# Optimization experiments

Measured on AMD Instinct MI355X. Metric: run time of the kernel, lower is better.

The kernel has to match this reference:

```python
import jax, jax.numpy as jnp
import numpy as np
from jax import lax

ANCHOR_AREAS = (128.0**2, 256.0**2, 512.0**2)
ASPECT_RATIOS = (0.5, 1.0, 2.0)
STRIDE = 32.0                      # resnet backbone: get_orig_stat maps fm -> input via x*32
PRE_NMS_TOP_N = 2000
POST_NMS_TOP_N = 100
NMS_IOU_T = 0.7
SCORE_T = 0.1
MIN_SCALE = 0.01
BBOX_XFORM_CLIP = float(np.log(1000.0 / 16.0))


def make_anchors(H, W):
    # anchors laid out in (H, W, A) order to match the offset permutation below
    sizes = []
    for area in ANCHOR_AREAS:
        for r in ASPECT_RATIOS:          # aspect_ratio = w / h
            sizes.append((np.sqrt(area * r), np.sqrt(area / r)))
    sizes = jnp.asarray(np.asarray(sizes, dtype=np.float32))  # [A, 2] (w, h)
    cy = (jnp.arange(H, dtype=jnp.float32) + 0.5) * STRIDE
    cx = (jnp.arange(W, dtype=jnp.float32) + 0.5) * STRIDE
    cyg, cxg = jnp.meshgrid(cy, cx, indexing='ij')             # [H, W]
    cxg = cxg[:, :, None]
    cyg = cyg[:, :, None]
    w = sizes[:, 0]
    h = sizes[:, 1]
    anchors = jnp.stack([cxg - w / 2, cyg - h / 2, cxg + w / 2, cyg + h / 2], axis=-1)
    return anchors.reshape(-1, 4)                              # [H*W*A, 4] xyxy


def decode_boxes(anchors, offsets):
    # anchors [N,4], offsets [B,N,4] (tx, ty, tw, th) -> boxes [B,N,4] xyxy
    wa = anchors[:, 2] - anchors[:, 0]
    ha = anchors[:, 3] - anchors[:, 1]
    cxa = anchors[:, 0] + 0.5 * wa
    cya = anchors[:, 1] + 0.5 * ha
    tx, ty = offsets[..., 0], offsets[..., 1]
    tw = jnp.minimum(offsets[..., 2], BBOX_XFORM_CLIP)
    th = jnp.minimum(offsets[..., 3], BBOX_XFORM_CLIP)
    px = tx * wa + cxa
    py = ty * ha + cya
    pw = jnp.exp(tw) * wa
    ph = jnp.exp(th) * ha
    return jnp.stack([px - pw / 2, py - ph / 2, px + pw / 2, py + ph / 2], axis=-1)


def box_iou(a, b):
    area_a = (a[:, 2] - a[:, 0]) * (a[:, 3] - a[:, 1])
    area_b = (b[:, 2] - b[:, 0]) * (b[:, 3] - b[:, 1])
    lt = jnp.maximum(a[:, None, :2], b[None, :, :2])
    rb = jnp.minimum(a[:, None, 2:], b[None, :, 2:])
    wh = jnp.clip(rb - lt, 0.0)
    inter = wh[..., 0] * wh[..., 1]
    return inter / (area_a[:, None] + area_b[None, :] - inter + 1e-9)


def nms_single(boxes, scores):
    # boxes [P,4] sorted by descending score; invalid entries carry score -1
    P = boxes.shape[0]
    iou = box_iou(boxes, boxes)
    idx = jnp.arange(P)

    def body(i, keep):
        sup = (iou[i] > NMS_IOU_T) & (idx > i)
        return jnp.where(keep[i], keep & (~sup), keep)

    keep = lax.stop_gradient(lax.fori_loop(0, P, body, scores > 0.0))
    kept_scores = jnp.where(keep, scores, -1.0)
    top_s, top_i = lax.top_k(kept_scores, POST_NMS_TOP_N)
    return boxes[top_i], top_s


def rpn_forward(features, W1, b1, W2, b2, W3, b3):
    B, Cin, H, W = features.shape
    A = W3.shape[0]
    # 3x3 sliding conv + ReLU
    t = lax.conv_general_dilated(
        features, W1, window_strides=(1, 1), padding='SAME',
        dimension_numbers=('NCHW', 'OIHW', 'NCHW'))
    t = jax.nn.relu(t + b1[None, :, None, None])
    # 1x1 sibling heads as channel contractions
    offs = jnp.einsum('bchw,oc->bohw', t, W2) + b2[None, :, None, None]   # [B, A*4, H, W]
    logits = jnp.einsum('bchw,oc->bohw', t, W3) + b3[None, :, None, None]  # [B, A, H, W]
    # reorder to per-anchor layout (H, W, A)
    offs = offs.reshape(B, A, 4, H, W).transpose(0, 3, 4, 1, 2).reshape(B, -1, 4)
    scores = jax.nn.sigmoid(logits.transpose(0, 2, 3, 1).reshape(B, -1))  # [B, N]
    anchors = make_anchors(H, W)
    boxes = decode_boxes(anchors, offs)                                    # [B, N, 4]
    # clip to image boundary (handle_cross_boundary_boxes during testing)
    img_w, img_h = W * STRIDE, H * STRIDE
    boxes = jnp.stack([
        jnp.clip(boxes[..., 0], 0.0, img_w),
        jnp.clip(boxes[..., 1], 0.0, img_h),
        jnp.clip(boxes[..., 2], 0.0, img_w),
        jnp.clip(boxes[..., 3], 0.0, img_h)], axis=-1)
    # score-threshold + min-scale filtering
    bw = boxes[..., 2] - boxes[..., 0]
    bh = boxes[..., 3] - boxes[..., 1]
    valid = (scores >= SCORE_T) & (bw > MIN_SCALE * img_w) & (bh > MIN_SCALE * img_h)
    masked = jnp.where(valid, scores, -1.0)
    # pre-NMS top-k, then per-image NMS + post-NMS top-n
    top_s, top_i = lax.top_k(masked, PRE_NMS_TOP_N)                        # [B, P]
    top_boxes = jnp.take_along_axis(boxes, top_i[..., None], axis=1)       # [B, P, 4]
    out_boxes, out_scores = jax.vmap(nms_single)(top_boxes, top_s)
    return out_boxes, out_scores                                           # [B,100,4], [B,100]


def setup_inputs() -> dict:
    key = jax.random.key(0)
    ks = jax.random.split(key, 4)
    B, Cin, H, W = 8, 1024, 50, 50
    A = 9
    C = 512
    return {
        'features': jax.random.normal(ks[0], (B, Cin, H, W), jnp.float32),
        'W1': jax.random.normal(ks[1], (C, Cin, 3, 3), jnp.float32) * 0.01,
        'b1': jnp.zeros((C,), jnp.float32),
        'W2': jax.random.normal(ks[2], (A * 4, C), jnp.float32) * 0.01,
        'b2': jnp.zeros((A * 4,), jnp.float32),
        'W3': jax.random.normal(ks[3], (A, C), jnp.float32) * 0.01,
        'b3': jnp.zeros((A,), jnp.float32),
    }


def reference(features, W1, b1, W2, b2, W3, b3):
    return rpn_forward(features, W1, b1, W2, b2, W3, b3)
```

## Files before the change

### kernel.cpp

```cpp
#include <hip/hip_runtime.h>
#include <cstdint>

#define NB 8
#define CIN 1024
#define HDIM 50
#define WDIM 50
#define COUT 512
#define NA 9
#define NANCH (HDIM*WDIM*NA)
#define PRE_N 2000
#define POST_N 100

typedef __attribute__((ext_vector_type(8))) short bf16x8;
typedef __attribute__((ext_vector_type(4))) float f32x4;
typedef __attribute__((ext_vector_type(16))) float f32x16;
typedef __attribute__((ext_vector_type(8))) unsigned short ushort8v;

constexpr size_t TPLANE    = 20578304;
constexpr size_t OFF_TPH   = 0;
constexpr size_t OFF_TPL   = 20578304;
constexpr size_t OFF_BOXES = 41156608;
constexpr size_t OFF_KEYS  = 44036608;
constexpr size_t OFF_TBOX  = 45476608;
constexpr size_t OFF_TS    = 45732608;
constexpr size_t OFF_SUP   = 45796608;
constexpr size_t QDIM      = 2976;
constexpr size_t PLSTRIDE  = QDIM * 8;
constexpr size_t PPLANE    = 48758784;
constexpr size_t OFF_PH    = 49892864;
constexpr size_t OFF_PL    = OFF_PH + PPLANE;
constexpr size_t WPLANE    = 9437184;
constexpr size_t OFF_WH    = 147410432;
constexpr size_t OFF_WL    = OFF_WH + WPLANE;

__device__ __forceinline__ void split2bf16(float v, unsigned short &hi, unsigned short &lo) {
    unsigned int u = __float_as_uint(v);
    unsigned int r = u + 0x7FFFu + ((u >> 16) & 1u);
    hi = (unsigned short)(r >> 16);
    float hf = __uint_as_float(((unsigned int)hi) << 16);
    float lf = v - hf;
    unsigned int u2 = __float_as_uint(lf);
    unsigned int r2 = u2 + 0x7FFFu + ((u2 >> 16) & 1u);
    lo = (unsigned short)(r2 >> 16);
}

__device__ __forceinline__ void gl_lds(const unsigned short* g, unsigned short* l) {
    __builtin_amdgcn_global_load_lds(
        (const __attribute__((address_space(1))) unsigned int*)(const void*)g,
        (__attribute__((address_space(3))) unsigned int*)(void*)l,
        16, 0, 0);
}

__global__ __launch_bounds__(256) void prep_all(const float* __restrict__ f,
                                                const float* __restrict__ W1,
                                                unsigned short* __restrict__ Ph,
                                                unsigned short* __restrict__ Pl,
                                                unsigned short* __restrict__ Wh,
                                                unsigned short* __restrict__ Wl) {
    int blk = blockIdx.x;
    if (blk < 5952) {
        int id = blk * 256 + threadIdx.x;
        int q = id % (int)QDIM; int r = id / (int)QDIM;
        int cic = r % 64; int b = r / 64;
        int pp = q - 53;
        int rr = pp / 52, cc = pp - rr * 52;
        int h = rr - 1, w = cc - 1;
        bool inb = (pp >= 0) && (pp < 2704) && (h >= 0) && (h < HDIM) && (w >= 0) && (w < WDIM);
        ushort8v hv0, lv0, hv1, lv1;
#pragma unroll
        for (int j = 0; j < 16; ++j) {
            float v = 0.f;
            if (inb) v = f[(((size_t)b * CIN + cic * 16 + j) * HDIM + h) * WDIM + w];
            unsigned short hi, lo;
            split2bf16(v, hi, lo);
            if (j < 8) { hv0[j] = hi; lv0[j] = lo; }
            else       { hv1[j - 8] = hi; lv1[j - 8] = lo; }
        }
        size_t b0 = ((size_t)((b * 64 + cic) * 2 + 0)) * PLSTRIDE + (size_t)q * 8;
        size_t b1 = ((size_t)((b * 64 + cic) * 2 + 1)) * PLSTRIDE + (size_t)q * 8;
        *(ushort8v*)&Ph[b0] = hv0;
        *(ushort8v*)&Ph[b1] = hv1;
        *(ushort8v*)&Pl[b0] = lv0;
        *(ushort8v*)&Pl[b1] = lv1;
    } else {
        int id = (blk - 5952) * 256 + threadIdx.x;
        int co = id % 64; int r = id / 64;
        int cic = r % 64; int cot = r / 64;
        int cog = cot * 64 + co;
        const float* src = W1 + ((size_t)cog * CIN + cic * 16) * 9;
        float v[144];
#pragma unroll
        for (int i = 0; i < 36; ++i) {
            float4 x = ((const float4*)src)[i];
            v[i * 4 + 0] = x.x; v[i * 4 + 1] = x.y; v[i * 4 + 2] = x.z; v[i * 4 + 3] = x.w;
        }
#pragma unroll
        for (int tap = 0; tap < 9; ++tap) {
            ushort8v hv0, lv0, hv1, lv1;
#pragma unroll
            for (int j = 0; j < 16; ++j) {
                unsigned short hi, lo;
                split2bf16(v[j * 9 + tap], hi, lo);
                if (j < 8) { hv0[j] = hi; lv0[j] = lo; }
                else       { hv1[j - 8] = hi; lv1[j - 8] = lo; }
            }
            size_t base = (((size_t)(cot * 64 + cic) * 9 + tap) * 2) * 512;
            *(ushort8v*)&Wh[base + co * 8]       = hv0;
            *(ushort8v*)&Wh[base + 512 + co * 8] = hv1;
            *(ushort8v*)&Wl[base + co * 8]       = lv0;
            *(ushort8v*)&Wl[base + 512 + co * 8] = lv1;
        }
    }
}


#define LOADA(SET_, SRC_, TG_)                                                       \
    do {                                                                             \
        _Pragma("unroll") for (int tl_ = 0; tl_ < 3; ++tl_) {                        \
            const int dlt_ = ((TG_) - 1) * 52 + (tl_ - 1);                           \
            _Pragma("unroll") for (int jm_ = 0; jm_ < 2; ++jm_) {                    \
                int ad_ = ((wv * 2 + jm_) * 32 + lm + dlt_ + 53) * 8;                \
                SET_[tl_][jm_][0] = *(const bf16x8*)&(SRC_)[lk * 3072 + ad_];        \
                SET_[tl_][jm_][1] = *(const bf16x8*)&(SRC_)[(2 + lk) * 3072 + ad_];  \
            }                                                                        \
        }                                                                            \
    } while (0)

#define LOADB(B_, BB_, TL_)                                                          \
    do {                                                                             \
        _Pragma("unroll") for (int jn_ = 0; jn_ < 2; ++jn_) {                        \
            int bd_ = (TL_) * 1024 + lk * 512 + (jn_ * 32 + lm) * 8;                 \
            B_[jn_][0] = *(const bf16x8*)&(BB_)[bd_];                                \
            B_[jn_][1] = *(const bf16x8*)&(BB_)[3072 + bd_];                         \
        }                                                                            \
    } while (0)

#define MFMA12A(SET_, TL_, B_)                                                       \
    do {                                                                             \
        _Pragma("unroll") for (int s_ = 0; s_ < 3; ++s_)                             \
        _Pragma("unroll") for (int jm_ = 0; jm_ < 2; ++jm_)                          \
        _Pragma("unroll") for (int jn_ = 0; jn_ < 2; ++jn_) {                        \
            const bf16x8 &av_ = (s_ == 2) ? SET_[TL_][jm_][1] : SET_[TL_][jm_][0];   \
            const bf16x8 &bv_ = (s_ == 1) ? B_[jn_][1] : B_[jn_][0];                 \
            acc[jm_][jn_] = __builtin_amdgcn_mfma_f32_32x32x16_bf16(                 \
                av_, bv_, acc[jm_][jn_], 0, 0, 0);                                   \
        }                                                                            \
    } while (0)

#define PHASE(CUR_, NXT_, CIC_, TG_, PRESRC_, NTG_, STAGEON_)                        \
    do {                                                                             \
        const int bbuf_ = ((CIC_) + (TG_)) & 1;                                      \
        const unsigned short* bB_ = Bbase + bbuf_ * 6144;                            \
        if ((STAGEON_) || (TG_) < 2) {                                               \
            int cicb_ = ((TG_) == 2) ? (CIC_) + 1 : (CIC_);                          \
            int tgn_  = ((TG_) == 2) ? 0 : (TG_) + 1;                                \
            _Pragma("unroll") for (int j_ = 0; j_ < 3; ++j_)                         \
                stageB(bbuf_ ^ 1, cicb_, tgn_, wv * 3 + j_);                         \
        }                                                                            \
        if (STAGEON_) {                                                              \
            if ((TG_) == 0) {                                                        \
                _Pragma("unroll") for (int j_ = 0; j_ < 3; ++j_)                     \
                    stageA((((CIC_) & 1) ^ 1), (CIC_) + 1, wv * 3 + j_);             \
            } else if ((TG_) == 1) {                                                 \
                _Pragma("unroll") for (int j_ = 0; j_ < 2; ++j_)                     \
                    stageA((((CIC_) & 1) ^ 1), (CIC_) + 1, 12 + wv * 2 + j_);        \
            } else {                                                                 \
                stageA((((CIC_) & 1) ^ 1), (CIC_) + 1, 20 + wv);                     \
            }                                                                        \
        }                                                                            \
        bf16x8 b0_[2][2], b1_[2][2];                                                 \
        LOADB(b0_, bB_, 0);                                                          \
        __builtin_amdgcn_s_setprio(1);                                               \
        LOADB(b1_, bB_, 1);                                                          \
        MFMA12A(CUR_, 0, b0_);                                                       \
        LOADB(b0_, bB_, 2);                                                          \
        if ((STAGEON_) || (TG_) < 2) LOADA(NXT_, PRESRC_, NTG_);                     \
        MFMA12A(CUR_, 1, b1_);                                                       \
        MFMA12A(CUR_, 2, b0_);                                                       \
        __builtin_amdgcn_s_setprio(0);                                               \
        if (STAGEON_) {                                                              \
            const int nv_ = ((TG_) == 0) ? 6 : ((TG_) == 1) ? 5 : 4;                 \
            __builtin_amdgcn_sched_group_barrier(0x070, nv_, 0);                     \
            __builtin_amdgcn_sched_group_barrier(0x100, 8, 0);                       \
            _Pragma("unroll") for (int g_ = 0; g_ < 8; ++g_) {                       \
                __builtin_amdgcn_sched_group_barrier(0x008, 3, 0);                   \
                __builtin_amdgcn_sched_group_barrier(0x100, 2, 0);                   \
            }                                                                        \
            __builtin_amdgcn_sched_group_barrier(0x008, 12, 0);                      \
        }                                                                            \
        __syncthreads();                                                             \
    } while (0)

#define DO_CIC(CUR_, NXT_, CIC_, STAGEON_)                                           \
    do {                                                                             \
        const unsigned short* bAc_ = Abase + ((CIC_) & 1) * 12288;                   \
        const unsigned short* bAn_ = Abase + (((CIC_) & 1) ^ 1) * 12288;             \
        PHASE(CUR_, NXT_, CIC_, 0, bAc_, 1, STAGEON_);                               \
        PHASE(NXT_, CUR_, CIC_, 1, bAc_, 2, STAGEON_);                               \
        PHASE(CUR_, NXT_, CIC_, 2, bAn_, 0, STAGEON_);                               \
    } while (0)

__global__ __launch_bounds__(256, 2) void conv_mfma(const unsigned short* __restrict__ FPh,
                                                    const unsigned short* __restrict__ FPl,
                                                    const unsigned short* __restrict__ WPh,
                                                    const unsigned short* __restrict__ WPl,
                                                    const float* __restrict__ b1,
                                                    unsigned short* __restrict__ Tph,
                                                    unsigned short* __restrict__ Tpl) {
    extern __shared__ unsigned short smem[];
    unsigned short* const Abase = smem;
    unsigned short* const Bbase = smem + 24576;

    int blk = blockIdx.x;
    int logical = (blk & 7) * 88 + (blk >> 3);
    int cot = logical & 7;
    int ptile = (logical >> 3) % 11;
    int b = logical / 88;
    int co0 = cot * 64;
    int P0 = 32 + ptile * 256;

    int t = threadIdx.x, wv = t >> 6, ln = t & 63;
    int lm = ln & 31, lk = ln >> 5;

    f32x16 acc[2][2];
#pragma unroll
    for (int jm = 0; jm < 2; ++jm)
#pragma unroll
        for (int jn = 0; jn < 2; ++jn)
#pragma unroll
            for (int rg = 0; rg < 16; ++rg) acc[jm][jn][rg] = 0.f;

    auto stageA = [&](int buf, int cic, int ci) {
        int r = (ci < 20) ? (ci & 3) : (ci - 20);
        int s = (ci < 20) ? (ci >> 2) : 5;
        int hl = r >> 1, lkc = r & 1;
        const unsigned short* pl = hl ? FPl : FPh;
        const unsigned short* src = pl
            + ((size_t)((b * 64 + cic) * 2 + lkc)) * PLSTRIDE
            + (size_t)P0 * 8 + s * 512 + ln * 8;
        gl_lds(src, &Abase[buf * 12288 + r * 3072 + s * 512]);
    };
    auto stageB = [&](int buf, int cic, int tg, int c) {
        int hl = c / 6, j = c % 6;
        const unsigned short* pl = hl ? WPl : WPh;
        const unsigned short* src = pl + (size_t)(cot * 64 + cic) * 9216
            + (size_t)(tg * 6 + j) * 512 + ln * 8;
        gl_lds(src, &Bbase[buf * 6144 + hl * 3072 + j * 512]);
    };

#pragma unroll
    for (int k = 0; k < 9; ++k) {
        int id = wv * 9 + k;
        if (id < 24) stageA(0, 0, id);
        else         stageB(0, 0, 0, id - 24);
    }
    __syncthreads();

    bf16x8 aX[3][2][2], aY[3][2][2];
    LOADA(aX, Abase, 0);

#pragma unroll 1
    for (int cc = 0; cc < 31; ++cc) {
        DO_CIC(aX, aY, 2 * cc,     1);
        DO_CIC(aY, aX, 2 * cc + 1, 1);
    }
    DO_CIC(aX, aY, 62, 1);
    DO_CIC(aY, aX, 63, 0);

#pragma unroll
    for (int jn = 0; jn < 2; ++jn) {
        int co = co0 + jn * 32 + lm;
        float bv = b1[co];
#pragma unroll
        for (int jm = 0; jm < 2; ++jm) {
#pragma unroll
            for (int rg = 0; rg < 16; ++rg) {
                int mrow = (rg & 3) + 8 * (rg >> 2) + 4 * lk;
                int pp = P0 + (wv * 2 + jm) * 32 + mrow;
                int rr = pp / 52, cc = pp - rr * 52;
                int h = rr - 1, w = cc - 1;
                if ((unsigned)h < HDIM && (unsigned)w < WDIM) {
                    float v = fmaxf(acc[jm][jn][rg] + bv, 0.f);
                    unsigned short hi, lo;
                    split2bf16(v, hi, lo);
                    int px = b * 2500 + h * 50 + w;
                    size_t sa = (((((size_t)(px >> 7) * 16 + (co >> 5)) * 8 + ((px >> 4) & 7)) * 4
                                  + ((co >> 3) & 3)) * 16 + (px & 15)) * 8 + (co & 7);
                    Tph[sa] = hi;
                    Tpl[sa] = lo;
                }
            }
        }
    }
}

__global__ __launch_bounds__(256) void proj_decode_mfma(const unsigned short* __restrict__ Tph,
                                                        const unsigned short* __restrict__ Tpl,
                                                        const float* __restrict__ W2,
                                                        const float* __restrict__ b2,
                                                        const float* __restrict__ W3,
                                                        const float* __restrict__ b3,
                                                        float* __restrict__ boxes,
                                                        unsigned long long* __restrict__ keys) {
    __shared__ unsigned short sTh[4096], sTl[4096];
    __shared__ unsigned short sWh[1536], sWl[1536];
    __shared__ float pout[128 * 46];

    int blk = blockIdx.x;
    int px0 = blk * 128;
    int t = threadIdx.x, wv = t >> 6, ln = t & 63;
    int lm = ln & 15, q = ln >> 4;

    f32x4 acc[2][3];
#pragma unroll
    for (int jm = 0; jm < 2; ++jm)
#pragma unroll
        for (int nf = 0; nf < 3; ++nf) acc[jm][nf] = (f32x4){0.f, 0.f, 0.f, 0.f};

#pragma unroll 1
    for (int cc16 = 0; cc16 < 16; ++cc16) {
        __syncthreads();
        size_t base = ((size_t)blk * 16 + cc16) * 4096;
        if (wv == 0) {
#pragma unroll
            for (int s = 0; s < 4; ++s) gl_lds(Tph + base + s * 512 + ln * 8, &sTh[s * 512]);
        } else if (wv == 1) {
#pragma unroll
            for (int s = 4; s < 8; ++s) gl_lds(Tph + base + s * 512 + ln * 8, &sTh[s * 512]);
        } else if (wv == 2) {
#pragma unroll
            for (int s = 0; s < 4; ++s) gl_lds(Tpl + base + s * 512 + ln * 8, &sTl[s * 512]);
        } else {
#pragma unroll
            for (int s = 4; s < 8; ++s) gl_lds(Tpl + base + s * 512 + ln * 8, &sTl[s * 512]);
        }
        int c0 = cc16 * 32;
        for (int idx = t; idx < 1536; idx += 256) {
            int o = idx >> 5, ci = idx & 31;
            float v = 0.f;
            if (o < 36) v = W2[o * 512 + c0 + ci];
            else if (o < 45) v = W3[(o - 36) * 512 + c0 + ci];
            unsigned short hi, lo;
            split2bf16(v, hi, lo);
            int ad = (((o >> 4) * 4 + (ci >> 3)) * 16 + (o & 15)) * 8 + (ci & 7);
            sWh[ad] = hi; sWl[ad] = lo;
        }
        __syncthreads();

        bf16x8 a[2][2], bb[3][2];
#pragma unroll
        for (int jm = 0; jm < 2; ++jm) {
            int mf = wv * 2 + jm;
            int ad = ((mf * 4 + q) * 16 + lm) * 8;
            a[jm][0] = *(const bf16x8*)&sTh[ad];
            a[jm][1] = *(const bf16x8*)&sTl[ad];
        }
#pragma unroll
        for (int nf = 0; nf < 3; ++nf) {
            int ad = ((nf * 4 + q) * 16 + lm) * 8;
            bb[nf][0] = *(const bf16x8*)&sWh[ad];
            bb[nf][1] = *(const bf16x8*)&sWl[ad];
        }
#pragma unroll
        for (int jm = 0; jm < 2; ++jm)
#pragma unroll
            for (int nf = 0; nf < 3; ++nf) {
                acc[jm][nf] = __builtin_amdgcn_mfma_f32_16x16x32_bf16(a[jm][0], bb[nf][0], acc[jm][nf], 0, 0, 0);
                acc[jm][nf] = __builtin_amdgcn_mfma_f32_16x16x32_bf16(a[jm][0], bb[nf][1], acc[jm][nf], 0, 0, 0);
                acc[jm][nf] = __builtin_amdgcn_mfma_f32_16x16x32_bf16(a[jm][1], bb[nf][0], acc[jm][nf], 0, 0, 0);
            }
    }
    __syncthreads();
#pragma unroll
    for (int jm = 0; jm < 2; ++jm)
#pragma unroll
        for (int nf = 0; nf < 3; ++nf) {
            int o = nf * 16 + lm;
            if (o < 45) {
                float bias = (o < 36) ? b2[o] : b3[o - 36];
#pragma unroll
                for (int rg = 0; rg < 4; ++rg) {
                    int pxl = (wv * 2 + jm) * 16 + q * 4 + rg;
                    pout[pxl * 46 + o] = acc[jm][nf][rg] + bias;
                }
            }
        }
    __syncthreads();

    const float AW[9] = {90.50966799187809f, 128.0f, 181.01933598375618f,
                         181.01933598375618f, 256.0f, 362.03867196751236f,
                         362.03867196751236f, 512.0f, 724.0773439350247f};
    const float AH[9] = {181.01933598375618f, 128.0f, 90.50966799187809f,
                         362.03867196751236f, 256.0f, 181.01933598375618f,
                         724.0773439350247f, 512.0f, 362.03867196751236f};
    const float CLIPV = 4.135166556742356f;
    const float IMG = 1600.0f;

    for (int it = t; it < 128 * 9; it += 256) {
        int pxl = it / 9, a = it - pxl * 9;
        int pxg = px0 + pxl;
        if (pxg >= 20000) continue;
        int b = pxg / 2500, rem = pxg % 2500;
        int h = rem / 50, w = rem % 50;

        float tx = pout[pxl * 46 + a * 4 + 0];
        float ty = pout[pxl * 46 + a * 4 + 1];
        float tw = pout[pxl * 46 + a * 4 + 2];
        float th = pout[pxl * 46 + a * 4 + 3];
        float lg = pout[pxl * 46 + 36 + a];

        float s = 1.0f / (1.0f + expf(-lg));

        float cx = ((float)w + 0.5f) * 32.0f;
        float cy = ((float)h + 0.5f) * 32.0f;
        float x1a = cx - 0.5f * AW[a];
        float x2a = cx + 0.5f * AW[a];
        float y1a = cy - 0.5f * AH[a];
        float y2a = cy + 0.5f * AH[a];
        float waf = x2a - x1a;
        float haf = y2a - y1a;
        float cxa = x1a + 0.5f * waf;
        float cya = y1a + 0.5f * haf;

        float twc = tw < CLIPV ? tw : CLIPV;
        float thc = th < CLIPV ? th : CLIPV;
        float pxc = tx * waf + cxa;
        float pyc = ty * haf + cya;
        float pw  = expf(twc) * waf;
        float ph  = expf(thc) * haf;

        float x1 = pxc - 0.5f * pw;
        float y1 = pyc - 0.5f * ph;
        float x2 = pxc + 0.5f * pw;
        float y2 = pyc + 0.5f * ph;
        x1 = fminf(fmaxf(x1, 0.f), IMG);
        y1 = fminf(fmaxf(y1, 0.f), IMG);
        x2 = fminf(fmaxf(x2, 0.f), IMG);
        y2 = fminf(fmaxf(y2, 0.f), IMG);

        float bw = x2 - x1, bh = y2 - y1;
        bool valid = (s >= 0.1f) && (bw > 16.0f) && (bh > 16.0f);
        float m = valid ? s : -1.0f;

        int idx = (h * WDIM + w) * NA + a;
        size_t gi = (size_t)b * NANCH + idx;
        ((float4*)boxes)[gi] = make_float4(x1, y1, x2, y2);
        unsigned int u = __float_as_uint(m);
        unsigned int k32 = (u & 0x80000000u) ? ~u : (u | 0x80000000u);
        keys[gi] = ((unsigned long long)k32 << 15) | (unsigned long long)(32767 - idx);
    }
}

__global__ __launch_bounds__(1024) void select_sort_kernel(const unsigned long long* __restrict__ keys,
                                                           const float* __restrict__ boxes,
                                                           float* __restrict__ top_boxes,
                                                           float* __restrict__ top_s) {
    int b = blockIdx.x;
    int t = threadIdx.x;
    int wv = t >> 6;
    const unsigned long long* kb = keys + (size_t)b * NANCH;

    __shared__ unsigned int whist[16][256];
    __shared__ unsigned int hist[256];
    __shared__ int s_chosen, s_rnew, s_done;
    __shared__ unsigned int s_cnt;
    __shared__ unsigned long long skeys[2048];

    const int widths[6] = {8, 8, 8, 8, 8, 7};
    unsigned long long prefix = 0;
    int bitsdone = 0;
    int r = PRE_N;

    if (t == 0) s_done = 0;

    for (int p = 0; p < 6; ++p) {
        int width = widths[p];
        int bins = 1 << width;
        int shift = 47 - bitsdone - width;
        for (int i = t; i < 16 * 256; i += 1024) ((unsigned int*)whist)[i] = 0;
        __syncthreads();
        for (int i = t; i < NANCH; i += 1024) {
            unsigned long long k = kb[i];
            if ((k >> (47 - bitsdone)) == prefix)
                atomicAdd(&whist[wv][(unsigned)((k >> shift) & (unsigned long long)(bins - 1))], 1u);
        }
        __syncthreads();
        if (t < bins) {
            unsigned int s = 0;
#pragma unroll
            for (int w = 0; w < 16; ++w) s += whist[w][t];
            hist[t] = s;
        }
        __syncthreads();
        if (t == 0) {
            int acc = 0, chosen = 0, rnew = 1;
            for (int d = bins - 1; d >= 0; --d) {
                int hv = (int)hist[d];
                if (acc + hv >= r) {
                    chosen = d; rnew = r - acc;
                    if ((PRE_N - r) + acc + hv <= 2048) s_done = 1;
                    break;
                }
                acc += hv;
            }
            s_chosen = chosen;
            s_rnew = rnew;
        }
        __syncthreads();
        prefix = (prefix << width) | (unsigned long long)s_chosen;
        bitsdone += width;
        r = s_rnew;
        __syncthreads();
        if (s_done) break;
    }
    unsigned long long Kst = prefix << (47 - bitsdone);

    if (t == 0) s_cnt = 0;
    __syncthreads();
    for (int i = t; i < NANCH; i += 1024) {
        unsigned long long k = kb[i];
        if (k >= Kst) {
            unsigned int p = atomicAdd(&s_cnt, 1u);
            if (p < 2048) skeys[p] = k;
        }
    }
    __syncthreads();
    unsigned int cnt = s_cnt;
    for (int i = t; i < 2048; i += 1024)
        if (i >= (int)cnt) skeys[i] = 0ull;
    for (int k = 2; k <= 2048; k <<= 1) {
        for (int j = k >> 1; j > 0; j >>= 1) {
            __syncthreads();
            for (int i = t; i < 2048; i += 1024) {
                int l = i ^ j;
                if (l > i) {
                    unsigned long long a = skeys[i], c = skeys[l];
                    bool up = ((i & k) == 0);
                    if (up ? (a < c) : (a > c)) { skeys[i] = c; skeys[l] = a; }
                }
            }
        }
    }
    __syncthreads();
    for (int i = t; i < PRE_N; i += 1024) {
        unsigned long long k = skeys[i];
        unsigned int k32 = (unsigned int)(k >> 15);
        float m = (k32 & 0x80000000u) ? __uint_as_float(k32 & 0x7FFFFFFFu)
                                      : __uint_as_float(~k32);
        unsigned int idx = 32767u - (unsigned int)(k & 32767ull);
        size_t gi = (size_t)b * NANCH + idx;
        top_s[b * PRE_N + i] = m;
        ((float4*)top_boxes)[b * PRE_N + i] = ((const float4*)boxes)[gi];
    }
}

__global__ __launch_bounds__(256) void sup_kernel(const float* __restrict__ top_boxes,
                                                  unsigned long long* __restrict__ supm) {
    int blk = blockIdx.x;
    int b = blk / 125;
    int chunk = blk % 125;
    int t = threadIdx.x;

    __shared__ float bx1[PRE_N], by1[PRE_N], bx2[PRE_N], by2[PRE_N];
    for (int i = t; i < PRE_N; i += 256) {
        float4 v = ((const float4*)top_boxes)[b * PRE_N + i];
        bx1[i] = v.x; by1[i] = v.y; bx2[i] = v.z; by2[i] = v.w;
    }
    __syncthreads();

    int wave = t >> 6, lane = t & 63;
    for (int rr = 0; rr < 4; ++rr) {
        int i = chunk * 16 + wave * 4 + rr;
        float ax1 = bx1[i], ay1 = by1[i], ax2 = bx2[i], ay2 = by2[i];
        float aarea = (ax2 - ax1) * (ay2 - ay1);
        for (int jw = 0; jw < 32; ++jw) {
            int j = jw * 64 + lane;
            bool sup = false;
            if (j > i && j < PRE_N) {
                float jx1 = bx1[j], jy1 = by1[j], jx2 = bx2[j], jy2 = by2[j];
                float ix1 = fmaxf(ax1, jx1), iy1 = fmaxf(ay1, jy1);
                float ix2 = fminf(ax2, jx2), iy2 = fminf(ay2, jy2);
                float iw = fmaxf(ix2 - ix1, 0.f);
                float ih = fmaxf(iy2 - iy1, 0.f);
                float inter = iw * ih;
                float barea = (jx2 - jx1) * (jy2 - jy1);
                float iou = inter / (aarea + barea - inter + 1e-9f);
                sup = iou > 0.7f;
            }
            unsigned long long m = __ballot(sup);
            if (lane == 0) supm[((size_t)b * PRE_N + i) * 32 + jw] = m;
        }
    }
}

__global__ __launch_bounds__(256) void nms_fin_kernel(const float* __restrict__ top_s,
                                                      const unsigned long long* __restrict__ supm,
                                                      const float* __restrict__ top_boxes,
                                                      float* __restrict__ out) {
    int b = blockIdx.x;
    int t = threadIdx.x;
    __shared__ unsigned int kw[64];
    __shared__ int wpre[65];

    if (t < 64) {
        int lane = t;
        unsigned int alive = 0;
        for (int q = 0; q < 32; ++q) {
            int i = lane * 32 + q;
            if (i < PRE_N && top_s[b * PRE_N + i] > 0.f) alive |= (1u << q);
        }
        const unsigned long long* sm = supm + (size_t)b * PRE_N * 32;
        const unsigned int* sup32 = (const unsigned int*)sm;

        for (int tt = 0; tt < 32; ++tt) {
            unsigned int alo = __shfl(alive, 2 * tt);
            unsigned int ahi = __shfl(alive, 2 * tt + 1);
            unsigned long long talive = (unsigned long long)alo | ((unsigned long long)ahi << 32);
            int i_row = tt * 64 + lane;
            unsigned long long rm = (i_row < PRE_N) ? sm[(size_t)i_row * 32 + tt] : 0ull;

            unsigned long long kept = 0, rem = talive;
            while (rem) {
                int j = __builtin_ctzll(rem);
                kept |= (1ull << j);
                unsigned long long rmj = __shfl(rm, j);
                rem &= ~rmj;
                rem &= ~(1ull << j);
            }

            unsigned int oracc = 0;
            unsigned long long kk = kept;
            while (kk) {
                int j0 = __builtin_ctzll(kk); kk &= kk - 1;
                int j1 = -1, j2 = -1, j3 = -1, j4 = -1, j5 = -1, j6 = -1, j7 = -1;
                if (kk) { j1 = __builtin_ctzll(kk); kk &= kk - 1; }
                if (kk) { j2 = __builtin_ctzll(kk); kk &= kk - 1; }
                if (kk) { j3 = __builtin_ctzll(kk); kk &= kk - 1; }
                if (kk) { j4 = __builtin_ctzll(kk); kk &= kk - 1; }
                if (kk) { j5 = __builtin_ctzll(kk); kk &= kk - 1; }
                if (kk) { j6 = __builtin_ctzll(kk); kk &= kk - 1; }
                if (kk) { j7 = __builtin_ctzll(kk); kk &= kk - 1; }
                unsigned int v0 = sup32[(size_t)(tt * 64 + j0) * 64 + lane];
                unsigned int v1 = (j1 >= 0) ? sup32[(size_t)(tt * 64 + j1) * 64 + lane] : 0u;
                unsigned int v2 = (j2 >= 0) ? sup32[(size_t)(tt * 64 + j2) * 64 + lane] : 0u;
                unsigned int v3 = (j3 >= 0) ? sup32[(size_t)(tt * 64 + j3) * 64 + lane] : 0u;
                unsigned int v4 = (j4 >= 0) ? sup32[(size_t)(tt * 64 + j4) * 64 + lane] : 0u;
                unsigned int v5 = (j5 >= 0) ? sup32[(size_t)(tt * 64 + j5) * 64 + lane] : 0u;
                unsigned int v6 = (j6 >= 0) ? sup32[(size_t)(tt * 64 + j6) * 64 + lane] : 0u;
                unsigned int v7 = (j7 >= 0) ? sup32[(size_t)(tt * 64 + j7) * 64 + lane] : 0u;
                oracc |= (v0 | v1) | (v2 | v3) | (v4 | v5) | (v6 | v7);
            }
            alive &= ~oracc;
            if (lane == 2 * tt)     alive = (unsigned int)kept;
            if (lane == 2 * tt + 1) alive = (unsigned int)(kept >> 32);
        }
        kw[lane] = alive;
    }
    __syncthreads();
    if (t == 0) {
        int run = 0;
        for (int w = 0; w < 64; ++w) { wpre[w] = run; run += __popc(kw[w]); }
        wpre[64] = run;
    }
    __syncthreads();
    int total = wpre[64];
    float* out_boxes  = out;
    float* out_scores = out + NB * POST_N * 4;
    for (int i = t; i < PRE_N; i += 256) {
        unsigned int w = kw[i >> 5];
        bool kept = (w >> (i & 31)) & 1u;
        int rk = wpre[i >> 5] + __popc(w & ((1u << (i & 31)) - 1u));
        int pos = kept ? rk : total + (i - rk);
        if (pos < POST_N) {
            out_scores[b * POST_N + pos] = kept ? top_s[b * PRE_N + i] : -1.0f;
            ((float4*)out_boxes)[b * POST_N + pos] = ((const float4*)top_boxes)[b * PRE_N + i];
        }
    }
}

extern "C" void kernel_launch(void* const* d_in, const int* in_sizes, int n_in,
                              void* d_out, int out_size, void* d_ws, size_t ws_size,
                              hipStream_t stream) {
    const float* features = (const float*)d_in[0];
    const float* W1 = (const float*)d_in[1];
    const float* b1 = (const float*)d_in[2];
    const float* W2 = (const float*)d_in[3];
    const float* b2 = (const float*)d_in[4];
    const float* W3 = (const float*)d_in[5];
    const float* b3 = (const float*)d_in[6];
    float* out = (float*)d_out;
    char* ws = (char*)d_ws;

    unsigned short* Tph = (unsigned short*)(ws + OFF_TPH);
    unsigned short* Tpl = (unsigned short*)(ws + OFF_TPL);
    float* boxes   = (float*)(ws + OFF_BOXES);
    unsigned long long* keys = (unsigned long long*)(ws + OFF_KEYS);
    float* top_boxes = (float*)(ws + OFF_TBOX);
    float* top_s     = (float*)(ws + OFF_TS);
    unsigned long long* supm = (unsigned long long*)(ws + OFF_SUP);
    unsigned short* FPh = (unsigned short*)(ws + OFF_PH);
    unsigned short* FPl = (unsigned short*)(ws + OFF_PL);
    unsigned short* WPh = (unsigned short*)(ws + OFF_WH);
    unsigned short* WPl = (unsigned short*)(ws + OFF_WL);

    static bool conv_attr_set = false;
    if (!conv_attr_set) {
        hipFuncSetAttribute(reinterpret_cast<const void*>(&conv_mfma),
                            hipFuncAttributeMaxDynamicSharedMemorySize, 73728);
        conv_attr_set = true;
    }

    prep_all<<<6080, 256, 0, stream>>>(features, W1, FPh, FPl, WPh, WPl);
    conv_mfma<<<704, 256, 73728, stream>>>(FPh, FPl, WPh, WPl, b1, Tph, Tpl);
    proj_decode_mfma<<<157, 256, 0, stream>>>(Tph, Tpl, W2, b2, W3, b3, boxes, keys);
    select_sort_kernel<<<NB, 1024, 0, stream>>>(keys, boxes, top_boxes, top_s);
    sup_kernel<<<NB * 125, 256, 0, stream>>>(top_boxes, supm);
    nms_fin_kernel<<<NB, 256, 0, stream>>>(top_s, supm, top_boxes, out);
}
```

Baseline: 973.7 us.

## Pre-split projection weights in prep kernel and unroll selection scan loops

The W2/W3 bf16 hi/lo split and swizzle move out of the per-tile loop of the projection kernel into extra blocks of the prep kernel. Each projection tile then loads its weights with async global-to-LDS copies instead of converting them again. Separately, the select kernel's histogram and gather scans are unrolled four-way to keep more loads in flight, and the NMS alive-mask read is vectorised to float4. The weight buffer reuses the suppression-matrix workspace region, which is safe only because the projection kernel reads it before sup_kernel writes there.

```diff
diff --git a/kernel.cpp b/kernel.cpp
--- a/kernel.cpp
+++ b/kernel.cpp
@@ -24,6 +24,8 @@
 constexpr size_t OFF_TBOX  = 45476608;
 constexpr size_t OFF_TS    = 45732608;
 constexpr size_t OFF_SUP   = 45796608;
+constexpr size_t OFF_W23H  = OFF_SUP;
+constexpr size_t OFF_W23L  = OFF_SUP + 49152;
 constexpr size_t QDIM      = 2976;
 constexpr size_t PLSTRIDE  = QDIM * 8;
 constexpr size_t PPLANE    = 48758784;
@@ -53,10 +55,14 @@
 
 __global__ __launch_bounds__(256) void prep_all(const float* __restrict__ f,
                                                 const float* __restrict__ W1,
+                                                const float* __restrict__ W2,
+                                                const float* __restrict__ W3,
                                                 unsigned short* __restrict__ Ph,
                                                 unsigned short* __restrict__ Pl,
                                                 unsigned short* __restrict__ Wh,
-                                                unsigned short* __restrict__ Wl) {
+                                                unsigned short* __restrict__ Wl,
+                                                unsigned short* __restrict__ W23h,
+                                                unsigned short* __restrict__ W23l) {
     int blk = blockIdx.x;
     if (blk < 5952) {
         int id = blk * 256 + threadIdx.x;
@@ -82,7 +88,7 @@
         *(ushort8v*)&Ph[b1] = hv1;
         *(ushort8v*)&Pl[b0] = lv0;
         *(ushort8v*)&Pl[b1] = lv1;
-    } else {
+    } else if (blk < 6080) {
         int id = (blk - 5952) * 256 + threadIdx.x;
         int co = id % 64; int r = id / 64;
         int cic = r % 64; int cot = r / 64;
@@ -109,6 +115,20 @@
             *(ushort8v*)&Wh[base + 512 + co * 8] = hv1;
             *(ushort8v*)&Wl[base + co * 8]       = lv0;
             *(ushort8v*)&Wl[base + 512 + co * 8] = lv1;
+        }
+    } else {
+        int id = (blk - 6080) * 256 + threadIdx.x;
+        for (int e = id; e < 48 * 512; e += 8 * 256) {
+            int o = e >> 9, c = e & 511;
+            float v = 0.f;
+            if (o < 36) v = W2[o * 512 + c];
+            else if (o < 45) v = W3[(o - 36) * 512 + c];
+            unsigned short hi, lo;
+            split2bf16(v, hi, lo);
+            int cc16 = c >> 5, ci = c & 31;
+            int ad = cc16 * 1536 + (((o >> 4) * 4 + (ci >> 3)) * 16 + (o & 15)) * 8 + (ci & 7);
+            W23h[ad] = hi;
+            W23l[ad] = lo;
         }
     }
 }
@@ -296,9 +316,9 @@
 
 __global__ __launch_bounds__(256) void proj_decode_mfma(const unsigned short* __restrict__ Tph,
                                                         const unsigned short* __restrict__ Tpl,
-                                                        const float* __restrict__ W2,
+                                                        const unsigned short* __restrict__ W23h,
+                                                        const unsigned short* __restrict__ W23l,
                                                         const float* __restrict__ b2,
-                                                        const float* __restrict__ W3,
                                                         const float* __restrict__ b3,
                                                         float* __restrict__ boxes,
                                                         unsigned long long* __restrict__ keys) {
@@ -324,26 +344,19 @@
         if (wv == 0) {
 #pragma unroll
             for (int s = 0; s < 4; ++s) gl_lds(Tph + base + s * 512 + ln * 8, &sTh[s * 512]);
+#pragma unroll
+            for (int s = 0; s < 3; ++s) gl_lds(W23h + cc16 * 1536 + s * 512 + ln * 8, &sWh[s * 512]);
         } else if (wv == 1) {
 #pragma unroll
             for (int s = 4; s < 8; ++s) gl_lds(Tph + base + s * 512 + ln * 8, &sTh[s * 512]);
         } else if (wv == 2) {
 #pragma unroll
             for (int s = 0; s < 4; ++s) gl_lds(Tpl + base + s * 512 + ln * 8, &sTl[s * 512]);
+#pragma unroll
+            for (int s = 0; s < 3; ++s) gl_lds(W23l + cc16 * 1536 + s * 512 + ln * 8, &sWl[s * 512]);
         } else {
 #pragma unroll
             for (int s = 4; s < 8; ++s) gl_lds(Tpl + base + s * 512 + ln * 8, &sTl[s * 512]);
-        }
-        int c0 = cc16 * 32;
-        for (int idx = t; idx < 1536; idx += 256) {
-            int o = idx >> 5, ci = idx & 31;
-            float v = 0.f;
-            if (o < 36) v = W2[o * 512 + c0 + ci];
-            else if (o < 45) v = W3[(o - 36) * 512 + c0 + ci];
-            unsigned short hi, lo;
-            split2bf16(v, hi, lo);
-            int ad = (((o >> 4) * 4 + (ci >> 3)) * 16 + (o & 15)) * 8 + (ci & 7);
-            sWh[ad] = hi; sWl[ad] = lo;
         }
         __syncthreads();
 
@@ -479,10 +492,21 @@
         int shift = 47 - bitsdone - width;
         for (int i = t; i < 16 * 256; i += 1024) ((unsigned int*)whist)[i] = 0;
         __syncthreads();
-        for (int i = t; i < NANCH; i += 1024) {
-            unsigned long long k = kb[i];
-            if ((k >> (47 - bitsdone)) == prefix)
-                atomicAdd(&whist[wv][(unsigned)((k >> shift) & (unsigned long long)(bins - 1))], 1u);
+        int sh = 47 - bitsdone;
+        for (int i0 = t; i0 < NANCH; i0 += 4096) {
+            int i1 = i0 + 1024, i2 = i0 + 2048, i3 = i0 + 3072;
+            unsigned long long k0 = kb[i0];
+            unsigned long long k1 = kb[i1 < NANCH ? i1 : 0];
+            unsigned long long k2 = kb[i2 < NANCH ? i2 : 0];
+            unsigned long long k3 = kb[i3 < NANCH ? i3 : 0];
+            if ((k0 >> sh) == prefix)
+                atomicAdd(&whist[wv][(unsigned)((k0 >> shift) & (unsigned long long)(bins - 1))], 1u);
+            if (i1 < NANCH && (k1 >> sh) == prefix)
+                atomicAdd(&whist[wv][(unsigned)((k1 >> shift) & (unsigned long long)(bins - 1))], 1u);
+            if (i2 < NANCH && (k2 >> sh) == prefix)
+                atomicAdd(&whist[wv][(unsigned)((k2 >> shift) & (unsigned long long)(bins - 1))], 1u);
+            if (i3 < NANCH && (k3 >> sh) == prefix)
+                atomicAdd(&whist[wv][(unsigned)((k3 >> shift) & (unsigned long long)(bins - 1))], 1u);
         }
         __syncthreads();
         if (t < bins) {
@@ -517,11 +541,27 @@
 
     if (t == 0) s_cnt = 0;
     __syncthreads();
-    for (int i = t; i < NANCH; i += 1024) {
-        unsigned long long k = kb[i];
-        if (k >= Kst) {
+    for (int i0 = t; i0 < NANCH; i0 += 4096) {
+        int i1 = i0 + 1024, i2 = i0 + 2048, i3 = i0 + 3072;
+        unsigned long long k0 = kb[i0];
+        unsigned long long k1 = kb[i1 < NANCH ? i1 : 0];
+        unsigned long long k2 = kb[i2 < NANCH ? i2 : 0];
+        unsigned long long k3 = kb[i3 < NANCH ? i3 : 0];
+        if (k0 >= Kst) {
             unsigned int p = atomicAdd(&s_cnt, 1u);
-            if (p < 2048) skeys[p] = k;
+            if (p < 2048) skeys[p] = k0;
+        }
+        if (i1 < NANCH && k1 >= Kst) {
+            unsigned int p = atomicAdd(&s_cnt, 1u);
+            if (p < 2048) skeys[p] = k1;
+        }
+        if (i2 < NANCH && k2 >= Kst) {
+            unsigned int p = atomicAdd(&s_cnt, 1u);
+            if (p < 2048) skeys[p] = k2;
+        }
+        if (i3 < NANCH && k3 >= Kst) {
+            unsigned int p = atomicAdd(&s_cnt, 1u);
+            if (p < 2048) skeys[p] = k3;
         }
     }
     __syncthreads();
@@ -605,9 +645,15 @@
     if (t < 64) {
         int lane = t;
         unsigned int alive = 0;
-        for (int q = 0; q < 32; ++q) {
-            int i = lane * 32 + q;
-            if (i < PRE_N && top_s[b * PRE_N + i] > 0.f) alive |= (1u << q);
+        const float* ts = top_s + (size_t)b * PRE_N + lane * 32;
+#pragma unroll
+        for (int q4 = 0; q4 < 8; ++q4) {
+            float4 v = *(const float4*)&ts[q4 * 4];
+            int base = lane * 32 + q4 * 4;
+            if (base + 0 < PRE_N && v.x > 0.f) alive |= 1u << (q4 * 4 + 0);
+            if (base + 1 < PRE_N && v.y > 0.f) alive |= 1u << (q4 * 4 + 1);
+            if (base + 2 < PRE_N && v.z > 0.f) alive |= 1u << (q4 * 4 + 2);
+            if (base + 3 < PRE_N && v.w > 0.f) alive |= 1u << (q4 * 4 + 3);
         }
         const unsigned long long* sm = supm + (size_t)b * PRE_N * 32;
         const unsigned int* sup32 = (const unsigned int*)sm;
@@ -702,6 +748,8 @@
     unsigned short* FPl = (unsigned short*)(ws + OFF_PL);
     unsigned short* WPh = (unsigned short*)(ws + OFF_WH);
     unsigned short* WPl = (unsigned short*)(ws + OFF_WL);
+    unsigned short* W23h = (unsigned short*)(ws + OFF_W23H);
+    unsigned short* W23l = (unsigned short*)(ws + OFF_W23L);
 
     static bool conv_attr_set = false;
     if (!conv_attr_set) {
@@ -710,9 +758,9 @@
         conv_attr_set = true;
     }
 
-    prep_all<<<6080, 256, 0, stream>>>(features, W1, FPh, FPl, WPh, WPl);
+    prep_all<<<6088, 256, 0, stream>>>(features, W1, W2, W3, FPh, FPl, WPh, WPl, W23h, W23l);
     conv_mfma<<<704, 256, 73728, stream>>>(FPh, FPl, WPh, WPl, b1, Tph, Tpl);
-    proj_decode_mfma<<<157, 256, 0, stream>>>(Tph, Tpl, W2, b2, W3, b3, boxes, keys);
+    proj_decode_mfma<<<157, 256, 0, stream>>>(Tph, Tpl, W23h, W23l, b2, b3, boxes, keys);
     select_sort_kernel<<<NB, 1024, 0, stream>>>(keys, boxes, top_boxes, top_s);
     sup_kernel<<<NB * 125, 256, 0, stream>>>(top_boxes, supm);
     nms_fin_kernel<<<NB, 256, 0, stream>>>(top_s, supm, top_boxes, out);
```

New measurement: 936.2 us. -3.8%, faster.
